# Kernel optimization log

Measured on AMD Instinct MI355X. Metric: run time of the kernel, lower is better.

The kernel has to match this reference:

```python
import jax, jax.numpy as jnp
import numpy as np

N, IN, OUT, R, E = 20000, 768, 768, 8, 320000


def setup_inputs() -> dict:
    key = jax.random.key(0)
    ks = jax.random.split(key, 9)
    x = jax.random.normal(ks[0], (N, IN), dtype=jnp.float32)
    edge_index = jax.random.randint(ks[1], (2, E), 0, N, dtype=jnp.int64)
    edge_type = jax.random.randint(ks[2], (E,), 0, R, dtype=jnp.int64)
    s1 = 1.0 / np.sqrt(IN)
    s2 = 1.0 / np.sqrt(OUT)
    W1 = jax.random.normal(ks[3], (R, IN, OUT), dtype=jnp.float32) * s1
    root1 = jax.random.normal(ks[4], (IN, OUT), dtype=jnp.float32) * s1
    b1 = jnp.zeros((OUT,), dtype=jnp.float32)
    W2 = jax.random.normal(ks[5], (R, OUT, OUT), dtype=jnp.float32) * s2
    root2 = jax.random.normal(ks[6], (OUT, OUT), dtype=jnp.float32) * s2
    b2 = jnp.zeros((OUT,), dtype=jnp.float32)
    return {"x": x, "edge_index": edge_index, "edge_type": edge_type,
            "W1": W1, "root1": root1, "b1": b1,
            "W2": W2, "root2": root2, "b2": b2}


def _rgcn_conv(x, src, dst, etype, W, root, b):
    # PyG RGCNConv: per-relation mean aggregation of neighbor features,
    # then relation-specific linear transform, plus root weight and bias.
    # mean(x_j @ W_r) == mean(x_j) @ W_r, so aggregate first, transform after.
    num_nodes = x.shape[0]
    num_rel = W.shape[0]
    x_src = x[src]                                  # [E, d_in]
    seg = dst * num_rel + etype                     # composite (node, relation) id
    sums = jax.ops.segment_sum(x_src, seg, num_segments=num_nodes * num_rel)
    cnt = jax.ops.segment_sum(jnp.ones((src.shape[0],), dtype=x.dtype), seg,
                              num_segments=num_nodes * num_rel)
    mean = sums / jnp.maximum(cnt, 1.0)[:, None]    # [N*R, d_in]
    mean = mean.reshape(num_nodes, num_rel, -1)     # [N, R, d_in]
    out = jnp.einsum('nri,rio->no', mean, W)        # relation-batched matmul
    return out + x @ root + b


def reference(x, edge_index, edge_type, W1, root1, b1, W2, root2, b2):
    src, dst = edge_index[0], edge_index[1]
    h = _rgcn_conv(x, src, dst, edge_type, W1, root1, b1)
    h = jax.nn.relu(h)
    out = _rgcn_conv(h, src, dst, edge_type, W2, root2, b2)
    return out
```

## Files before the change

kernel.cpp:

```cpp
#include <hip/hip_runtime.h>
#include <hip/hip_bf16.h>
#include <stdint.h>

#define N_NODES 20000
#define DIM     768
#define NREL    8
#define NEDGE   320000
#define NSEG    (N_NODES * NREL)
#define GKA     6144
#define GK      6912
#define NT_TILES (GK / 64)
#define NPW     2

typedef short short8 __attribute__((ext_vector_type(8)));
typedef float f32x4  __attribute__((ext_vector_type(4)));

__device__ __forceinline__ void async_load16(const void* g, void* l) {
  __builtin_amdgcn_global_load_lds((const __attribute__((address_space(1))) void*)g,
                                   (__attribute__((address_space(3))) void*)l,
                                   16, 0, 0);
}

__device__ __forceinline__ int imin(int a, int b) { return a < b ? a : b; }

__device__ __forceinline__ float bf_lo(uint32_t v) {
  return __builtin_bit_cast(float, v << 16);
}
__device__ __forceinline__ float bf_hi(uint32_t v) {
  return __builtin_bit_cast(float, v & 0xffff0000u);
}
__device__ __forceinline__ uint32_t pack_bf16x2(float a, float b) {
  uint32_t lo = __builtin_bit_cast(unsigned short, __float2bfloat16(a));
  uint32_t hi = __builtin_bit_cast(unsigned short, __float2bfloat16(b));
  return lo | (hi << 16);
}

__global__ void seg_count_kernel(const int* __restrict__ dst, const int* __restrict__ et,
                                 int* __restrict__ segcnt, int e_cnt) {
  int e = blockIdx.x * 256 + threadIdx.x;
  if (e < e_cnt) atomicAdd(&segcnt[dst[e] * NREL + et[e]], 1);
}

__global__ void block_scan_kernel(const int* __restrict__ in, int* __restrict__ out,
                                  int* __restrict__ partials, int n) {
  __shared__ int wsum[16];
  const int t = threadIdx.x, lane = t & 63, wave = t >> 6;
  const int i = blockIdx.x * 1024 + t;
  int v = (i < n) ? in[i] : 0;
  int s = v;
#pragma unroll
  for (int off = 1; off < 64; off <<= 1) {
    int u = __shfl_up(s, off, 64);
    if (lane >= off) s += u;
  }
  if (lane == 63) wsum[wave] = s;
  __syncthreads();
  if (t < 16) {
    int w = wsum[t];
#pragma unroll
    for (int off = 1; off < 16; off <<= 1) {
      int u = __shfl_up(w, off, 64);
      if (t >= off) w += u;
    }
    wsum[t] = w;
  }
  __syncthreads();
  const int basew = (wave > 0) ? wsum[wave - 1] : 0;
  if (i < n) out[i] = basew + s - v;
  if (t == 1023) partials[blockIdx.x] = wsum[15];
}

__global__ void partial_scan_kernel(int* __restrict__ partials, int nb) {
  const int lane = threadIdx.x & 63;
  int carry = 0;
  for (int base = 0; base < nb; base += 64) {
    const int i = base + lane;
    int v = (i < nb) ? partials[i] : 0;
    int s = v;
#pragma unroll
    for (int off = 1; off < 64; off <<= 1) {
      int u = __shfl_up(s, off, 64);
      if (lane >= off) s += u;
    }
    if (i < nb) partials[i] = carry + s - v;
    carry += __shfl(s, 63, 64);
  }
}

__global__ void add_offsets_kernel(int* __restrict__ soffs, const int* __restrict__ partials,
                                   int* __restrict__ cursor, int n) {
  const int i = blockIdx.x * 1024 + threadIdx.x;
  if (i < n) {
    const int v = soffs[i] + partials[blockIdx.x];
    soffs[i] = v;
    cursor[i] = v;
  }
  if (i == 0) soffs[n] = NEDGE;
}

__global__ void seg_scatter_kernel(const int* __restrict__ src, const int* __restrict__ dst,
                                   const int* __restrict__ et, int* __restrict__ cursor,
                                   int* __restrict__ es, int e_cnt) {
  int e = blockIdx.x * 256 + threadIdx.x;
  if (e < e_cnt) {
    const int seg = dst[e] * NREL + et[e];
    const int p = atomicAdd(&cursor[seg], 1);
    es[p] = src[e];
  }
}

__global__ void cvt_bf16_kernel(const float4* __restrict__ in, ushort4* __restrict__ out, int n4) {
  int i = blockIdx.x * 256 + threadIdx.x;
  if (i < n4) {
    float4 f = in[i];
    ushort4 r;
    r.x = __builtin_bit_cast(unsigned short, __float2bfloat16(f.x));
    r.y = __builtin_bit_cast(unsigned short, __float2bfloat16(f.y));
    r.z = __builtin_bit_cast(unsigned short, __float2bfloat16(f.z));
    r.w = __builtin_bit_cast(unsigned short, __float2bfloat16(f.w));
    out[i] = r;
  }
}

__global__ void transpose_w_kernel(const float* __restrict__ src, __hip_bfloat16* __restrict__ dst,
                                   int rows, int col_off) {
  __shared__ float tile[32][33];
  const int c0 = blockIdx.x * 32;
  const int r0 = blockIdx.y * 32;
  const int tx = threadIdx.x, ty = threadIdx.y;
  for (int i = ty; i < 32; i += 8) {
    int r = r0 + i, c = c0 + tx;
    tile[i][tx] = (r < rows) ? src[(size_t)r * DIM + c] : 0.f;
  }
  __syncthreads();
  for (int i = ty; i < 32; i += 8) {
    int c = c0 + i, r = r0 + tx;
    if (r < rows)
      dst[(size_t)c * GK + col_off + r] = __float2bfloat16(tile[tx][i]);
  }
}

__global__ __launch_bounds__(256) void aggregate_kernel(
    const __hip_bfloat16* __restrict__ feat,
    const int* __restrict__ soffs, const int* __restrict__ es,
    __hip_bfloat16* __restrict__ Abuf,
    int node_base, int rows) {
  const int t = threadIdx.x;
  const int lane = t & 63;
  const int wave = t >> 6;
  const int boff = lane * 8;

  int nloc = (blockIdx.x * 4 + wave) * NPW;
  for (int it = 0; it < NPW; ++it, ++nloc) {
    if (nloc >= rows) return;
    const int n = node_base + nloc;
    char* Ab = (char*)(Abuf + (size_t)nloc * GK);
#pragma unroll
    for (int r = 0; r < NREL; ++r) {
      const int beg = soffs[n * NREL + r], end = soffs[n * NREL + r + 1];
      float acc[12];
#pragma unroll
      for (int i = 0; i < 12; ++i) acc[i] = 0.f;
      int e = beg;
      for (; e + 2 <= end; e += 2) {
        const int s0 = es[e], s1 = es[e + 1];
        const char* p0 = (const char*)(feat + (size_t)s0 * DIM) + boff;
        const char* p1 = (const char*)(feat + (size_t)s1 * DIM) + boff;
        const uint2 a0 = *(const uint2*)(p0);
        const uint2 a1 = *(const uint2*)(p0 + 512);
        const uint2 a2 = *(const uint2*)(p0 + 1024);
        const uint2 b0 = *(const uint2*)(p1);
        const uint2 b1 = *(const uint2*)(p1 + 512);
        const uint2 b2 = *(const uint2*)(p1 + 1024);
        acc[0]  += bf_lo(a0.x); acc[1]  += bf_hi(a0.x);
        acc[2]  += bf_lo(a0.y); acc[3]  += bf_hi(a0.y);
        acc[4]  += bf_lo(a1.x); acc[5]  += bf_hi(a1.x);
        acc[6]  += bf_lo(a1.y); acc[7]  += bf_hi(a1.y);
        acc[8]  += bf_lo(a2.x); acc[9]  += bf_hi(a2.x);
        acc[10] += bf_lo(a2.y); acc[11] += bf_hi(a2.y);
        acc[0]  += bf_lo(b0.x); acc[1]  += bf_hi(b0.x);
        acc[2]  += bf_lo(b0.y); acc[3]  += bf_hi(b0.y);
        acc[4]  += bf_lo(b1.x); acc[5]  += bf_hi(b1.x);
        acc[6]  += bf_lo(b1.y); acc[7]  += bf_hi(b1.y);
        acc[8]  += bf_lo(b2.x); acc[9]  += bf_hi(b2.x);
        acc[10] += bf_lo(b2.y); acc[11] += bf_hi(b2.y);
      }
      if (e < end) {
        const int s0 = es[e];
        const char* p0 = (const char*)(feat + (size_t)s0 * DIM) + boff;
        const uint2 a0 = *(const uint2*)(p0);
        const uint2 a1 = *(const uint2*)(p0 + 512);
        const uint2 a2 = *(const uint2*)(p0 + 1024);
        acc[0]  += bf_lo(a0.x); acc[1]  += bf_hi(a0.x);
        acc[2]  += bf_lo(a0.y); acc[3]  += bf_hi(a0.y);
        acc[4]  += bf_lo(a1.x); acc[5]  += bf_hi(a1.x);
        acc[6]  += bf_lo(a1.y); acc[7]  += bf_hi(a1.y);
        acc[8]  += bf_lo(a2.x); acc[9]  += bf_hi(a2.x);
        acc[10] += bf_lo(a2.y); acc[11] += bf_hi(a2.y);
      }
      const float inv = 1.f / fmaxf((float)(end - beg), 1.f);
      uint2 o0, o1, o2;
      o0.x = pack_bf16x2(acc[0] * inv, acc[1] * inv);
      o0.y = pack_bf16x2(acc[2] * inv, acc[3] * inv);
      o1.x = pack_bf16x2(acc[4] * inv, acc[5] * inv);
      o1.y = pack_bf16x2(acc[6] * inv, acc[7] * inv);
      o2.x = pack_bf16x2(acc[8] * inv, acc[9] * inv);
      o2.y = pack_bf16x2(acc[10] * inv, acc[11] * inv);
      char* dst = Ab + r * (DIM * 2);
      *(uint2*)(dst + boff) = o0;
      *(uint2*)(dst + boff + 512) = o1;
      *(uint2*)(dst + boff + 1024) = o2;
    }
    const char* fsrc = (const char*)(feat + (size_t)n * DIM);
    char* fdst = Ab + GKA * 2;
    *(uint2*)(fdst + boff) = *(const uint2*)(fsrc + boff);
    *(uint2*)(fdst + boff + 512) = *(const uint2*)(fsrc + boff + 512);
    *(uint2*)(fdst + boff + 1024) = *(const uint2*)(fsrc + boff + 1024);
  }
}

__global__ __launch_bounds__(512, 2) void gemm_kernel(
    const __hip_bfloat16* __restrict__ A,
    const __hip_bfloat16* __restrict__ BT,
    const float* __restrict__ bias,
    __hip_bfloat16* __restrict__ outb,
    float* __restrict__ outf,
    int mvalid, int node_base, int mode) {
  __shared__ __hip_bfloat16 lds[2][2][2][128][64];

  const int t = threadIdx.x;
  const int lane = t & 63;
  const int wid = t >> 6;
  const int wave_m = wid >> 2;
  const int wave_n = wid & 3;
  const int ml = lane & 15;
  const int quad = lane >> 4;
  const int sw8 = ml & 7;
  const int lsub = lane >> 3;
  const int lg = (lane & 7) ^ lsub;
  const int wrow = wid * 8;

  const int nbx = gridDim.x;
  const int nwg = nbx * gridDim.y;
  const int lid = blockIdx.y * nbx + blockIdx.x;
  const int q = nwg >> 3, r = nwg & 7;
  const int xcd = lid & 7, off = lid >> 3;
  const int swz = (xcd < r ? xcd * (q + 1) : r * (q + 1) + (xcd - r) * q) + off;
  const int m0 = (swz / nbx) * 256;
  const int n0 = (swz % nbx) * 256;

  const char* cA = (const char*)A;
  const char* cB = (const char*)BT;
  uint32_t offA[2][2], offB[2][2];
#pragma unroll
  for (int h = 0; h < 2; ++h)
#pragma unroll
    for (int i = 0; i < 2; ++i) {
      const int srow = h * 128 + i * 64 + wrow + lsub;
      const int ar = imin(m0 + srow, mvalid - 1);
      offA[h][i] = (uint32_t)ar * (uint32_t)(GK * 2) + (uint32_t)(lg * 16);
      offB[h][i] = (uint32_t)(n0 + srow) * (uint32_t)(GK * 2) + (uint32_t)(lg * 16);
    }

#define VMCNT(N) asm volatile("s_waitcnt vmcnt(" #N ")" ::: "memory")
#define BAR()    asm volatile("s_barrier" ::: "memory")

#define STG_A(SB, H, TS) do {                                                      \
    const char* _p = cA + (size_t)(TS) * 128;                                      \
    async_load16(_p + offA[H][0], &lds[SB][0][H][wrow][0]);                        \
    async_load16(_p + offA[H][1], &lds[SB][0][H][64 + wrow][0]);                   \
  } while (0)

#define STG_B(SB, H, TS) do {                                                      \
    const char* _p = cB + (size_t)(TS) * 128;                                      \
    async_load16(_p + offB[H][0], &lds[SB][1][H][wrow][0]);                        \
    async_load16(_p + offB[H][1], &lds[SB][1][H][64 + wrow][0]);                   \
  } while (0)

#define LOAD_A(BUF, MH, DST)                                                       \
  _Pragma("unroll") for (int mi = 0; mi < 4; ++mi)                                 \
  _Pragma("unroll") for (int kk = 0; kk < 2; ++kk)                                 \
    DST[mi][kk] = *(const short8*)&lds[BUF][0][MH][wave_m * 64 + mi * 16 + ml]     \
                                                 [((kk * 4 + quad) ^ sw8) * 8];

#define LOAD_B(BUF, NH, DST)                                                       \
  _Pragma("unroll") for (int ni = 0; ni < 2; ++ni)                                 \
  _Pragma("unroll") for (int kk = 0; kk < 2; ++kk)                                 \
    DST[ni][kk] = *(const short8*)&lds[BUF][1][NH][wave_n * 32 + ni * 16 + ml]     \
                                                 [((kk * 4 + quad) ^ sw8) * 8];

#define DO_MFMA(MH, NH, AF, BF)                                                    \
  _Pragma("unroll") for (int mi = 0; mi < 4; ++mi)                                 \
  _Pragma("unroll") for (int ni = 0; ni < 2; ++ni) {                               \
    acc[MH][NH][mi][ni] = __builtin_amdgcn_mfma_f32_16x16x32_bf16(                 \
        AF[mi][0], BF[ni][0], acc[MH][NH][mi][ni], 0, 0, 0);                       \
    acc[MH][NH][mi][ni] = __builtin_amdgcn_mfma_f32_16x16x32_bf16(                 \
        AF[mi][1], BF[ni][1], acc[MH][NH][mi][ni], 0, 0, 0);                       \
  }

  f32x4 acc[2][2][4][2] = {};
  short8 aA[4][2], aB[4][2];
  short8 b0[2][2], b1[2][2];

  STG_A(0, 0, 0); STG_B(0, 0, 0);
  STG_B(0, 1, 0);
  STG_A(0, 1, 0);
  STG_A(1, 0, 1); STG_B(1, 0, 1);
  STG_B(1, 1, 1);
  STG_A(1, 1, 1);
  VMCNT(12);
  BAR();
  LOAD_A(0, 0, aA);
  LOAD_B(0, 0, b0);
  VMCNT(8);
  BAR();

  for (int T = 0; T < NT_TILES; ++T) {
    const int buf = T & 1;
    const int ts2 = (T + 2 < NT_TILES) ? T + 2 : NT_TILES - 1;
    VMCNT(8);
    LOAD_B(buf, 1, b1);
    BAR();
    __builtin_amdgcn_s_setprio(1);
    DO_MFMA(0, 0, aA, b0);
    __builtin_amdgcn_s_setprio(0);
    BAR();
    VMCNT(4);
    STG_A(buf, 0, ts2);
    STG_B(buf, 0, ts2);
    LOAD_A(buf, 1, aB);
    BAR();
    __builtin_amdgcn_s_setprio(1);
    DO_MFMA(0, 1, aA, b1);
    __builtin_amdgcn_s_setprio(0);
    BAR();
    STG_B(buf, 1, ts2);
    LOAD_A(buf ^ 1, 0, aA);
    BAR();
    __builtin_amdgcn_s_setprio(1);
    DO_MFMA(1, 0, aB, b0);
    __builtin_amdgcn_s_setprio(0);
    BAR();
    VMCNT(8);
    STG_A(buf, 1, ts2);
    LOAD_B(buf ^ 1, 0, b0);
    BAR();
    __builtin_amdgcn_s_setprio(1);
    DO_MFMA(1, 1, aB, b1);
    __builtin_amdgcn_s_setprio(0);
    BAR();
  }
  VMCNT(0);

#undef VMCNT
#undef BAR
#undef STG_A
#undef STG_B
#undef LOAD_A
#undef LOAD_B
#undef DO_MFMA

  float bcol[2][2];
#pragma unroll
  for (int nh = 0; nh < 2; ++nh)
#pragma unroll
    for (int ni = 0; ni < 2; ++ni)
      bcol[nh][ni] = bias[n0 + nh * 128 + wave_n * 32 + ni * 16 + ml];

#pragma unroll
  for (int mh = 0; mh < 2; ++mh)
#pragma unroll
    for (int mi = 0; mi < 4; ++mi)
#pragma unroll
      for (int rr = 0; rr < 4; ++rr) {
        const int row = m0 + mh * 128 + wave_m * 64 + mi * 16 + quad * 4 + rr;
        if (row < mvalid) {
          const size_t orow = (size_t)(node_base + row) * DIM;
#pragma unroll
          for (int nh = 0; nh < 2; ++nh)
#pragma unroll
            for (int ni = 0; ni < 2; ++ni) {
              const int col = n0 + nh * 128 + wave_n * 32 + ni * 16 + ml;
              const float v = acc[mh][nh][mi][ni][rr] + bcol[nh][ni];
              if (mode == 0) outb[orow + col] = __float2bfloat16(fmaxf(v, 0.f));
              else           outf[orow + col] = v;
            }
        }
      }
}

extern "C" void kernel_launch(void* const* d_in, const int* in_sizes, int n_in,
                              void* d_out, int out_size, void* d_ws, size_t ws_size,
                              hipStream_t stream) {
  const float* x     = (const float*)d_in[0];
  const int*   eidx  = (const int*)d_in[1];
  const int*   etype = (const int*)d_in[2];
  const float* W1    = (const float*)d_in[3];
  const float* root1 = (const float*)d_in[4];
  const float* b1    = (const float*)d_in[5];
  const float* W2    = (const float*)d_in[6];
  const float* root2 = (const float*)d_in[7];
  const float* b2    = (const float*)d_in[8];
  float* out = (float*)d_out;
  const int* esrc_in = eidx;
  const int* edst_in = eidx + NEDGE;

  char* p = (char*)d_ws;
  auto alloc = [&](size_t bytes) -> char* {
    char* r = p;
    p += (bytes + 255) & ~(size_t)255;
    return r;
  };
  __hip_bfloat16* xb  = (__hip_bfloat16*)alloc((size_t)N_NODES * DIM * 2);
  __hip_bfloat16* hb  = (__hip_bfloat16*)alloc((size_t)N_NODES * DIM * 2);
  __hip_bfloat16* w1t = (__hip_bfloat16*)alloc((size_t)DIM * GK * 2);
  __hip_bfloat16* w2t = (__hip_bfloat16*)alloc((size_t)DIM * GK * 2);
  int* segcnt   = (int*)alloc((size_t)NSEG * 4);
  int* soffs    = (int*)alloc((size_t)(NSEG + 1) * 4);
  int* cursor   = (int*)alloc((size_t)NSEG * 4);
  int* partials = (int*)alloc(256 * 4);
  int* es       = (int*)alloc((size_t)NEDGE * 4);
  size_t used = (size_t)(p - (char*)d_ws);
  size_t remain = (ws_size > used) ? (ws_size - used) : 0;
  long long caprows_ll = (long long)(remain / ((size_t)GK * 2));
  int caprows = (int)((caprows_ll / 128) * 128);
  if (caprows > 20096) caprows = 20096;
  if (caprows < 128) caprows = 128;
  __hip_bfloat16* Abuf = (__hip_bfloat16*)p;

  const int NB = (NSEG + 1023) / 1024;
  hipMemsetAsync(segcnt, 0, (size_t)NSEG * 4, stream);
  seg_count_kernel<<<(NEDGE + 255) / 256, 256, 0, stream>>>(edst_in, etype, segcnt, NEDGE);
  block_scan_kernel<<<NB, 1024, 0, stream>>>(segcnt, soffs, partials, NSEG);
  partial_scan_kernel<<<1, 64, 0, stream>>>(partials, NB);
  add_offsets_kernel<<<NB, 1024, 0, stream>>>(soffs, partials, cursor, NSEG);
  seg_scatter_kernel<<<(NEDGE + 255) / 256, 256, 0, stream>>>(esrc_in, edst_in, etype, cursor, es, NEDGE);

  cvt_bf16_kernel<<<((N_NODES * DIM / 4) + 255) / 256, 256, 0, stream>>>(
      (const float4*)x, (ushort4*)xb, N_NODES * DIM / 4);
  dim3 tb(32, 8);
  transpose_w_kernel<<<dim3(DIM / 32, (NREL * DIM) / 32), tb, 0, stream>>>(W1, w1t, NREL * DIM, 0);
  transpose_w_kernel<<<dim3(DIM / 32, DIM / 32), tb, 0, stream>>>(root1, w1t, DIM, NREL * DIM);
  transpose_w_kernel<<<dim3(DIM / 32, (NREL * DIM) / 32), tb, 0, stream>>>(W2, w2t, NREL * DIM, 0);
  transpose_w_kernel<<<dim3(DIM / 32, DIM / 32), tb, 0, stream>>>(root2, w2t, DIM, NREL * DIM);

  for (int base = 0; base < N_NODES; base += caprows) {
    int rows = N_NODES - base; if (rows > caprows) rows = caprows;
    int agrid = (rows + 4 * NPW - 1) / (4 * NPW);
    aggregate_kernel<<<agrid, 256, 0, stream>>>(xb, soffs, es, Abuf, base, rows);
    dim3 grid(DIM / 256, (rows + 255) / 256);
    gemm_kernel<<<grid, 512, 0, stream>>>(Abuf, w1t, b1, hb, nullptr, rows, base, 0);
  }
  for (int base = 0; base < N_NODES; base += caprows) {
    int rows = N_NODES - base; if (rows > caprows) rows = caprows;
    int agrid = (rows + 4 * NPW - 1) / (4 * NPW);
    aggregate_kernel<<<agrid, 256, 0, stream>>>(hb, soffs, es, Abuf, base, rows);
    dim3 grid(DIM / 256, (rows + 255) / 256);
    gemm_kernel<<<grid, 512, 0, stream>>>(Abuf, w2t, b2, nullptr, out, rows, base, 1);
  }
}
```

Baseline: 1.124 ms.

## Transform features per relation first, then gather-mean the projected slabs

New measurement: 939.1 us. 1.2x faster.

```diff
diff --git a/kernel.cpp b/kernel.cpp
--- a/kernel.cpp
+++ b/kernel.cpp
@@ -7,9 +7,9 @@
 #define NREL    8
 #define NEDGE   320000
 #define NSEG    (N_NODES * NREL)
-#define GKA     6144
-#define GK      6912
-#define NT_TILES (GK / 64)
+#define NSLAB   9
+#define KDIM    768
+#define NKT     12
 #define NPW     2
 
 typedef short short8 __attribute__((ext_vector_type(8)));
@@ -21,7 +21,7 @@
                                    16, 0, 0);
 }
 
-__device__ __forceinline__ int imin(int a, int b) { return a < b ? a : b; }
+__host__ __device__ __forceinline__ int imin(int a, int b) { return a < b ? a : b; }
 
 __device__ __forceinline__ float bf_lo(uint32_t v) {
   return __builtin_bit_cast(float, v << 16);
@@ -122,110 +122,28 @@
   }
 }
 
-__global__ void transpose_w_kernel(const float* __restrict__ src, __hip_bfloat16* __restrict__ dst,
-                                   int rows, int col_off) {
+__global__ void transpose_w2_kernel(const float* __restrict__ W, const float* __restrict__ root,
+                                    __hip_bfloat16* __restrict__ dst) {
   __shared__ float tile[32][33];
+  const int s = blockIdx.z;
+  const float* src = (s < 8) ? (W + (size_t)s * DIM * DIM) : root;
   const int c0 = blockIdx.x * 32;
   const int r0 = blockIdx.y * 32;
   const int tx = threadIdx.x, ty = threadIdx.y;
-  for (int i = ty; i < 32; i += 8) {
-    int r = r0 + i, c = c0 + tx;
-    tile[i][tx] = (r < rows) ? src[(size_t)r * DIM + c] : 0.f;
-  }
+  for (int i = ty; i < 32; i += 8)
+    tile[i][tx] = src[(size_t)(r0 + i) * DIM + c0 + tx];
   __syncthreads();
   for (int i = ty; i < 32; i += 8) {
-    int c = c0 + i, r = r0 + tx;
-    if (r < rows)
-      dst[(size_t)c * GK + col_off + r] = __float2bfloat16(tile[tx][i]);
-  }
-}
-
-__global__ __launch_bounds__(256) void aggregate_kernel(
-    const __hip_bfloat16* __restrict__ feat,
-    const int* __restrict__ soffs, const int* __restrict__ es,
-    __hip_bfloat16* __restrict__ Abuf,
-    int node_base, int rows) {
-  const int t = threadIdx.x;
-  const int lane = t & 63;
-  const int wave = t >> 6;
-  const int boff = lane * 8;
-
-  int nloc = (blockIdx.x * 4 + wave) * NPW;
-  for (int it = 0; it < NPW; ++it, ++nloc) {
-    if (nloc >= rows) return;
-    const int n = node_base + nloc;
-    char* Ab = (char*)(Abuf + (size_t)nloc * GK);
-#pragma unroll
-    for (int r = 0; r < NREL; ++r) {
-      const int beg = soffs[n * NREL + r], end = soffs[n * NREL + r + 1];
-      float acc[12];
-#pragma unroll
-      for (int i = 0; i < 12; ++i) acc[i] = 0.f;
-      int e = beg;
-      for (; e + 2 <= end; e += 2) {
-        const int s0 = es[e], s1 = es[e + 1];
-        const char* p0 = (const char*)(feat + (size_t)s0 * DIM) + boff;
-        const char* p1 = (const char*)(feat + (size_t)s1 * DIM) + boff;
-        const uint2 a0 = *(const uint2*)(p0);
-        const uint2 a1 = *(const uint2*)(p0 + 512);
-        const uint2 a2 = *(const uint2*)(p0 + 1024);
-        const uint2 b0 = *(const uint2*)(p1);
-        const uint2 b1 = *(const uint2*)(p1 + 512);
-        const uint2 b2 = *(const uint2*)(p1 + 1024);
-        acc[0]  += bf_lo(a0.x); acc[1]  += bf_hi(a0.x);
-        acc[2]  += bf_lo(a0.y); acc[3]  += bf_hi(a0.y);
-        acc[4]  += bf_lo(a1.x); acc[5]  += bf_hi(a1.x);
-        acc[6]  += bf_lo(a1.y); acc[7]  += bf_hi(a1.y);
-        acc[8]  += bf_lo(a2.x); acc[9]  += bf_hi(a2.x);
-        acc[10] += bf_lo(a2.y); acc[11] += bf_hi(a2.y);
-        acc[0]  += bf_lo(b0.x); acc[1]  += bf_hi(b0.x);
-        acc[2]  += bf_lo(b0.y); acc[3]  += bf_hi(b0.y);
-        acc[4]  += bf_lo(b1.x); acc[5]  += bf_hi(b1.x);
-        acc[6]  += bf_lo(b1.y); acc[7]  += bf_hi(b1.y);
-        acc[8]  += bf_lo(b2.x); acc[9]  += bf_hi(b2.x);
-        acc[10] += bf_lo(b2.y); acc[11] += bf_hi(b2.y);
-      }
-      if (e < end) {
-        const int s0 = es[e];
-        const char* p0 = (const char*)(feat + (size_t)s0 * DIM) + boff;
-        const uint2 a0 = *(const uint2*)(p0);
-        const uint2 a1 = *(const uint2*)(p0 + 512);
-        const uint2 a2 = *(const uint2*)(p0 + 1024);
-        acc[0]  += bf_lo(a0.x); acc[1]  += bf_hi(a0.x);
-        acc[2]  += bf_lo(a0.y); acc[3]  += bf_hi(a0.y);
-        acc[4]  += bf_lo(a1.x); acc[5]  += bf_hi(a1.x);
-        acc[6]  += bf_lo(a1.y); acc[7]  += bf_hi(a1.y);
-        acc[8]  += bf_lo(a2.x); acc[9]  += bf_hi(a2.x);
-        acc[10] += bf_lo(a2.y); acc[11] += bf_hi(a2.y);
-      }
-      const float inv = 1.f / fmaxf((float)(end - beg), 1.f);
-      uint2 o0, o1, o2;
-      o0.x = pack_bf16x2(acc[0] * inv, acc[1] * inv);
-      o0.y = pack_bf16x2(acc[2] * inv, acc[3] * inv);
-      o1.x = pack_bf16x2(acc[4] * inv, acc[5] * inv);
-      o1.y = pack_bf16x2(acc[6] * inv, acc[7] * inv);
-      o2.x = pack_bf16x2(acc[8] * inv, acc[9] * inv);
-      o2.y = pack_bf16x2(acc[10] * inv, acc[11] * inv);
-      char* dst = Ab + r * (DIM * 2);
-      *(uint2*)(dst + boff) = o0;
-      *(uint2*)(dst + boff + 512) = o1;
-      *(uint2*)(dst + boff + 1024) = o2;
-    }
-    const char* fsrc = (const char*)(feat + (size_t)n * DIM);
-    char* fdst = Ab + GKA * 2;
-    *(uint2*)(fdst + boff) = *(const uint2*)(fsrc + boff);
-    *(uint2*)(fdst + boff + 512) = *(const uint2*)(fsrc + boff + 512);
-    *(uint2*)(fdst + boff + 1024) = *(const uint2*)(fsrc + boff + 1024);
+    const int o = c0 + i, ii = r0 + tx;
+    dst[((size_t)s * DIM + o) * KDIM + ii] = __float2bfloat16(tile[tx][i]);
   }
 }
 
 __global__ __launch_bounds__(512, 2) void gemm_kernel(
     const __hip_bfloat16* __restrict__ A,
     const __hip_bfloat16* __restrict__ BT,
-    const float* __restrict__ bias,
-    __hip_bfloat16* __restrict__ outb,
-    float* __restrict__ outf,
-    int mvalid, int node_base, int mode) {
+    __hip_bfloat16* __restrict__ Z,
+    int mvalid, int zcols) {
   __shared__ __hip_bfloat16 lds[2][2][2][128][64];
 
   const int t = threadIdx.x;
@@ -258,8 +176,8 @@
     for (int i = 0; i < 2; ++i) {
       const int srow = h * 128 + i * 64 + wrow + lsub;
       const int ar = imin(m0 + srow, mvalid - 1);
-      offA[h][i] = (uint32_t)ar * (uint32_t)(GK * 2) + (uint32_t)(lg * 16);
-      offB[h][i] = (uint32_t)(n0 + srow) * (uint32_t)(GK * 2) + (uint32_t)(lg * 16);
+      offA[h][i] = (uint32_t)ar * (uint32_t)(KDIM * 2) + (uint32_t)(lg * 16);
+      offB[h][i] = (uint32_t)(n0 + srow) * (uint32_t)(KDIM * 2) + (uint32_t)(lg * 16);
     }
 
 #define VMCNT(N) asm volatile("s_waitcnt vmcnt(" #N ")" ::: "memory")
@@ -315,9 +233,9 @@
   VMCNT(8);
   BAR();
 
-  for (int T = 0; T < NT_TILES; ++T) {
+  for (int T = 0; T < NKT; ++T) {
     const int buf = T & 1;
-    const int ts2 = (T + 2 < NT_TILES) ? T + 2 : NT_TILES - 1;
+    const int ts2 = (T + 2 < NKT) ? T + 2 : NKT - 1;
     VMCNT(8);
     LOAD_B(buf, 1, b1);
     BAR();
@@ -360,13 +278,6 @@
 #undef LOAD_B
 #undef DO_MFMA
 
-  float bcol[2][2];
-#pragma unroll
-  for (int nh = 0; nh < 2; ++nh)
-#pragma unroll
-    for (int ni = 0; ni < 2; ++ni)
-      bcol[nh][ni] = bias[n0 + nh * 128 + wave_n * 32 + ni * 16 + ml];
-
 #pragma unroll
   for (int mh = 0; mh < 2; ++mh)
 #pragma unroll
@@ -375,18 +286,151 @@
       for (int rr = 0; rr < 4; ++rr) {
         const int row = m0 + mh * 128 + wave_m * 64 + mi * 16 + quad * 4 + rr;
         if (row < mvalid) {
-          const size_t orow = (size_t)(node_base + row) * DIM;
+          const size_t orow = (size_t)row * (size_t)zcols;
 #pragma unroll
           for (int nh = 0; nh < 2; ++nh)
 #pragma unroll
             for (int ni = 0; ni < 2; ++ni) {
               const int col = n0 + nh * 128 + wave_n * 32 + ni * 16 + ml;
-              const float v = acc[mh][nh][mi][ni][rr] + bcol[nh][ni];
-              if (mode == 0) outb[orow + col] = __float2bfloat16(fmaxf(v, 0.f));
-              else           outf[orow + col] = v;
+              Z[orow + col] = __float2bfloat16(acc[mh][nh][mi][ni][rr]);
             }
         }
       }
+}
+
+__device__ __forceinline__ void seg_mean_add(const char* cZ, size_t zrb, uint32_t colb,
+                                             int beg, int end, int boff, float* acc,
+                                             const int* es) {
+  float s[12];
+#pragma unroll
+  for (int i = 0; i < 12; ++i) s[i] = 0.f;
+  int e = beg;
+  for (; e + 2 <= end; e += 2) {
+    const int s0 = es[e], s1 = es[e + 1];
+    const char* p0 = cZ + (size_t)s0 * zrb + colb + boff;
+    const char* p1 = cZ + (size_t)s1 * zrb + colb + boff;
+    const uint2 a0 = *(const uint2*)(p0);
+    const uint2 a1 = *(const uint2*)(p0 + 512);
+    const uint2 a2 = *(const uint2*)(p0 + 1024);
+    const uint2 c0 = *(const uint2*)(p1);
+    const uint2 c1 = *(const uint2*)(p1 + 512);
+    const uint2 c2 = *(const uint2*)(p1 + 1024);
+    s[0]  += bf_lo(a0.x); s[1]  += bf_hi(a0.x);
+    s[2]  += bf_lo(a0.y); s[3]  += bf_hi(a0.y);
+    s[4]  += bf_lo(a1.x); s[5]  += bf_hi(a1.x);
+    s[6]  += bf_lo(a1.y); s[7]  += bf_hi(a1.y);
+    s[8]  += bf_lo(a2.x); s[9]  += bf_hi(a2.x);
+    s[10] += bf_lo(a2.y); s[11] += bf_hi(a2.y);
+    s[0]  += bf_lo(c0.x); s[1]  += bf_hi(c0.x);
+    s[2]  += bf_lo(c0.y); s[3]  += bf_hi(c0.y);
+    s[4]  += bf_lo(c1.x); s[5]  += bf_hi(c1.x);
+    s[6]  += bf_lo(c1.y); s[7]  += bf_hi(c1.y);
+    s[8]  += bf_lo(c2.x); s[9]  += bf_hi(c2.x);
+    s[10] += bf_lo(c2.y); s[11] += bf_hi(c2.y);
+  }
+  if (e < end) {
+    const int s0 = es[e];
+    const char* p0 = cZ + (size_t)s0 * zrb + colb + boff;
+    const uint2 a0 = *(const uint2*)(p0);
+    const uint2 a1 = *(const uint2*)(p0 + 512);
+    const uint2 a2 = *(const uint2*)(p0 + 1024);
+    s[0]  += bf_lo(a0.x); s[1]  += bf_hi(a0.x);
+    s[2]  += bf_lo(a0.y); s[3]  += bf_hi(a0.y);
+    s[4]  += bf_lo(a1.x); s[5]  += bf_hi(a1.x);
+    s[6]  += bf_lo(a1.y); s[7]  += bf_hi(a1.y);
+    s[8]  += bf_lo(a2.x); s[9]  += bf_hi(a2.x);
+    s[10] += bf_lo(a2.y); s[11] += bf_hi(a2.y);
+  }
+  const float inv = 1.f / (float)(end - beg);
+#pragma unroll
+  for (int i = 0; i < 12; ++i) acc[i] += s[i] * inv;
+}
+
+__global__ __launch_bounds__(256) void aggregate2_kernel(
+    const __hip_bfloat16* __restrict__ Z,
+    int zcols,
+    const int* __restrict__ soffs, const int* __restrict__ es,
+    const float* __restrict__ bias,
+    float* __restrict__ accf,
+    __hip_bfloat16* __restrict__ outb,
+    int g0, int ns, int first, int last, int mode) {
+  const int t = threadIdx.x;
+  const int lane = t & 63;
+  const int wave = t >> 6;
+  const int boff = lane * 8;
+  const char* cZ = (const char*)Z;
+  const size_t zrb = (size_t)zcols * 2;
+
+  int n = (blockIdx.x * 4 + wave) * NPW;
+  for (int it = 0; it < NPW; ++it, ++n) {
+    if (n >= N_NODES) return;
+    float acc[12];
+    if (first) {
+      const float4 bv0 = *(const float4*)(bias + lane * 4);
+      const float4 bv1 = *(const float4*)(bias + 256 + lane * 4);
+      const float4 bv2 = *(const float4*)(bias + 512 + lane * 4);
+      acc[0] = bv0.x; acc[1] = bv0.y; acc[2] = bv0.z; acc[3] = bv0.w;
+      acc[4] = bv1.x; acc[5] = bv1.y; acc[6] = bv1.z; acc[7] = bv1.w;
+      acc[8] = bv2.x; acc[9] = bv2.y; acc[10] = bv2.z; acc[11] = bv2.w;
+    } else {
+      const float* ap = accf + (size_t)n * DIM;
+      const float4 v0 = *(const float4*)(ap + lane * 4);
+      const float4 v1 = *(const float4*)(ap + 256 + lane * 4);
+      const float4 v2 = *(const float4*)(ap + 512 + lane * 4);
+      acc[0] = v0.x; acc[1] = v0.y; acc[2] = v0.z; acc[3] = v0.w;
+      acc[4] = v1.x; acc[5] = v1.y; acc[6] = v1.z; acc[7] = v1.w;
+      acc[8] = v2.x; acc[9] = v2.y; acc[10] = v2.z; acc[11] = v2.w;
+    }
+    const int rend = imin(g0 + ns, NREL);
+    for (int r = g0; r < rend; ++r) {
+      const int beg = soffs[n * NREL + r], end = soffs[n * NREL + r + 1];
+      if (beg == end) continue;
+      seg_mean_add(cZ, zrb, (uint32_t)(r - g0) * (DIM * 2), beg, end, boff, acc, es);
+    }
+    if (last) {
+      const char* zr = cZ + (size_t)n * zrb + (size_t)(NSLAB - 1 - g0) * (DIM * 2);
+      const uint2 r0 = *(const uint2*)(zr + boff);
+      const uint2 r1 = *(const uint2*)(zr + boff + 512);
+      const uint2 r2 = *(const uint2*)(zr + boff + 1024);
+      acc[0] += bf_lo(r0.x); acc[1] += bf_hi(r0.x);
+      acc[2] += bf_lo(r0.y); acc[3] += bf_hi(r0.y);
+      acc[4] += bf_lo(r1.x); acc[5] += bf_hi(r1.x);
+      acc[6] += bf_lo(r1.y); acc[7] += bf_hi(r1.y);
+      acc[8] += bf_lo(r2.x); acc[9] += bf_hi(r2.x);
+      acc[10] += bf_lo(r2.y); acc[11] += bf_hi(r2.y);
+    }
+    if (!last) {
+      float* ap = accf + (size_t)n * DIM;
+      float4 v0, v1, v2;
+      v0.x = acc[0]; v0.y = acc[1]; v0.z = acc[2]; v0.w = acc[3];
+      v1.x = acc[4]; v1.y = acc[5]; v1.z = acc[6]; v1.w = acc[7];
+      v2.x = acc[8]; v2.y = acc[9]; v2.z = acc[10]; v2.w = acc[11];
+      *(float4*)(ap + lane * 4) = v0;
+      *(float4*)(ap + 256 + lane * 4) = v1;
+      *(float4*)(ap + 512 + lane * 4) = v2;
+    } else if (mode == 0) {
+      char* dst = (char*)outb + (size_t)n * (DIM * 2);
+      uint2 o0, o1, o2;
+      o0.x = pack_bf16x2(fmaxf(acc[0], 0.f), fmaxf(acc[1], 0.f));
+      o0.y = pack_bf16x2(fmaxf(acc[2], 0.f), fmaxf(acc[3], 0.f));
+      o1.x = pack_bf16x2(fmaxf(acc[4], 0.f), fmaxf(acc[5], 0.f));
+      o1.y = pack_bf16x2(fmaxf(acc[6], 0.f), fmaxf(acc[7], 0.f));
+      o2.x = pack_bf16x2(fmaxf(acc[8], 0.f), fmaxf(acc[9], 0.f));
+      o2.y = pack_bf16x2(fmaxf(acc[10], 0.f), fmaxf(acc[11], 0.f));
+      *(uint2*)(dst + boff) = o0;
+      *(uint2*)(dst + boff + 512) = o1;
+      *(uint2*)(dst + boff + 1024) = o2;
+    } else {
+      float* ap = accf + (size_t)n * DIM;
+      float4 v0, v1, v2;
+      v0.x = acc[0]; v0.y = acc[1]; v0.z = acc[2]; v0.w = acc[3];
+      v1.x = acc[4]; v1.y = acc[5]; v1.z = acc[6]; v1.w = acc[7];
+      v2.x = acc[8]; v2.y = acc[9]; v2.z = acc[10]; v2.w = acc[11];
+      *(float4*)(ap + lane * 4) = v0;
+      *(float4*)(ap + 256 + lane * 4) = v1;
+      *(float4*)(ap + 512 + lane * 4) = v2;
+    }
+  }
 }
 
 extern "C" void kernel_launch(void* const* d_in, const int* in_sizes, int n_in,
@@ -411,25 +455,25 @@
     p += (bytes + 255) & ~(size_t)255;
     return r;
   };
-  __hip_bfloat16* xb  = (__hip_bfloat16*)alloc((size_t)N_NODES * DIM * 2);
-  __hip_bfloat16* hb  = (__hip_bfloat16*)alloc((size_t)N_NODES * DIM * 2);
-  __hip_bfloat16* w1t = (__hip_bfloat16*)alloc((size_t)DIM * GK * 2);
-  __hip_bfloat16* w2t = (__hip_bfloat16*)alloc((size_t)DIM * GK * 2);
+  __hip_bfloat16* wt  = (__hip_bfloat16*)alloc((size_t)NSLAB * DIM * KDIM * 2);
   int* segcnt   = (int*)alloc((size_t)NSEG * 4);
   int* soffs    = (int*)alloc((size_t)(NSEG + 1) * 4);
   int* cursor   = (int*)alloc((size_t)NSEG * 4);
   int* partials = (int*)alloc(256 * 4);
   int* es       = (int*)alloc((size_t)NEDGE * 4);
-  size_t used = (size_t)(p - (char*)d_ws);
-  size_t remain = (ws_size > used) ? (ws_size - used) : 0;
-  long long caprows_ll = (long long)(remain / ((size_t)GK * 2));
-  int caprows = (int)((caprows_ll / 128) * 128);
-  if (caprows > 20096) caprows = 20096;
-  if (caprows < 128) caprows = 128;
-  __hip_bfloat16* Abuf = (__hip_bfloat16*)p;
+  __hip_bfloat16* xb  = (__hip_bfloat16*)alloc((size_t)N_NODES * DIM * 2);
+  __hip_bfloat16* hb  = xb;
+
+  const size_t used = (size_t)(p - (char*)d_ws);
+  const size_t remain = (ws_size > used) ? (ws_size - used) : 0;
+  const size_t slab_bytes = (size_t)N_NODES * DIM * 2;
+  int S = (int)(remain / slab_bytes);
+  if (S > NSLAB) S = NSLAB;
+  if (S < 1) S = 1;
+  __hip_bfloat16* Z = (__hip_bfloat16*)p;
 
   const int NB = (NSEG + 1023) / 1024;
-  hipMemsetAsync(segcnt, 0, (size_t)NSEG * 4, stream);
+  (void)hipMemsetAsync(segcnt, 0, (size_t)NSEG * 4, stream);
   seg_count_kernel<<<(NEDGE + 255) / 256, 256, 0, stream>>>(edst_in, etype, segcnt, NEDGE);
   block_scan_kernel<<<NB, 1024, 0, stream>>>(segcnt, soffs, partials, NSEG);
   partial_scan_kernel<<<1, 64, 0, stream>>>(partials, NB);
@@ -439,23 +483,27 @@
   cvt_bf16_kernel<<<((N_NODES * DIM / 4) + 255) / 256, 256, 0, stream>>>(
       (const float4*)x, (ushort4*)xb, N_NODES * DIM / 4);
   dim3 tb(32, 8);
-  transpose_w_kernel<<<dim3(DIM / 32, (NREL * DIM) / 32), tb, 0, stream>>>(W1, w1t, NREL * DIM, 0);
-  transpose_w_kernel<<<dim3(DIM / 32, DIM / 32), tb, 0, stream>>>(root1, w1t, DIM, NREL * DIM);
-  transpose_w_kernel<<<dim3(DIM / 32, (NREL * DIM) / 32), tb, 0, stream>>>(W2, w2t, NREL * DIM, 0);
-  transpose_w_kernel<<<dim3(DIM / 32, DIM / 32), tb, 0, stream>>>(root2, w2t, DIM, NREL * DIM);
-
-  for (int base = 0; base < N_NODES; base += caprows) {
-    int rows = N_NODES - base; if (rows > caprows) rows = caprows;
-    int agrid = (rows + 4 * NPW - 1) / (4 * NPW);
-    aggregate_kernel<<<agrid, 256, 0, stream>>>(xb, soffs, es, Abuf, base, rows);
-    dim3 grid(DIM / 256, (rows + 255) / 256);
-    gemm_kernel<<<grid, 512, 0, stream>>>(Abuf, w1t, b1, hb, nullptr, rows, base, 0);
-  }
-  for (int base = 0; base < N_NODES; base += caprows) {
-    int rows = N_NODES - base; if (rows > caprows) rows = caprows;
-    int agrid = (rows + 4 * NPW - 1) / (4 * NPW);
-    aggregate_kernel<<<agrid, 256, 0, stream>>>(hb, soffs, es, Abuf, base, rows);
-    dim3 grid(DIM / 256, (rows + 255) / 256);
-    gemm_kernel<<<grid, 512, 0, stream>>>(Abuf, w2t, b2, nullptr, out, rows, base, 1);
-  }
-}
+  transpose_w2_kernel<<<dim3(DIM / 32, DIM / 32, NSLAB), tb, 0, stream>>>(W1, root1, wt);
+
+  const int agrid = (N_NODES + 4 * NPW - 1) / (4 * NPW);
+
+  for (int g0 = 0; g0 < NSLAB; g0 += S) {
+    const int ns = imin(S, NSLAB - g0);
+    const int zc = ns * DIM;
+    dim3 gg(zc / 256, (N_NODES + 255) / 256);
+    gemm_kernel<<<gg, 512, 0, stream>>>(xb, wt + (size_t)g0 * DIM * KDIM, Z, N_NODES, zc);
+    aggregate2_kernel<<<agrid, 256, 0, stream>>>(Z, zc, soffs, es, b1, out, hb,
+                                                 g0, ns, g0 == 0, g0 + ns == NSLAB, 0);
+  }
+
+  transpose_w2_kernel<<<dim3(DIM / 32, DIM / 32, NSLAB), tb, 0, stream>>>(W2, root2, wt);
+
+  for (int g0 = 0; g0 < NSLAB; g0 += S) {
+    const int ns = imin(S, NSLAB - g0);
+    const int zc = ns * DIM;
+    dim3 gg(zc / 256, (N_NODES + 255) / 256);
+    gemm_kernel<<<gg, 512, 0, stream>>>(hb, wt + (size_t)g0 * DIM * KDIM, Z, N_NODES, zc);
+    aggregate2_kernel<<<agrid, 256, 0, stream>>>(Z, zc, soffs, es, b2, out, nullptr,
+                                                 g0, ns, g0 == 0, g0 + ns == NSLAB, 1);
+  }
+}
```
